# Performance work log

Hardware: AMD Instinct MI355X
Metric: run time of the kernel (lower is better)

## Reference

```python
import jax, jax.numpy as jnp
import numpy as np

NUM_HEADS = 8
EMBED_DIM = 512
HEAD_SIZE = EMBED_DIM // NUM_HEADS
B, S = 4, 2048


def setup_inputs() -> dict:
    key = jax.random.key(0)
    ks = jax.random.split(key, 9)
    scale = 1.0 / np.sqrt(HEAD_SIZE)
    return {
        "values": jax.random.normal(ks[0], (B, S, EMBED_DIM), jnp.float32),
        "keys": jax.random.normal(ks[1], (B, S, EMBED_DIM), jnp.float32),
        "query": jax.random.normal(ks[2], (B, S, EMBED_DIM), jnp.float32),
        "mask": jax.random.randint(ks[3], (B, S), 0, 2, jnp.int32),
        # per-head projection weights, nn.Linear convention: y = x @ W.T, W is [out,in]
        "Wv": jax.random.normal(ks[4], (HEAD_SIZE, HEAD_SIZE), jnp.float32) * scale,
        "Wk": jax.random.normal(ks[5], (HEAD_SIZE, HEAD_SIZE), jnp.float32) * scale,
        "Wq": jax.random.normal(ks[6], (HEAD_SIZE, HEAD_SIZE), jnp.float32) * scale,
        "Wo": jax.random.normal(ks[7], (EMBED_DIM, EMBED_DIM), jnp.float32) * (1.0 / np.sqrt(EMBED_DIM)),
        "bo": jax.random.normal(ks[8], (EMBED_DIM,), jnp.float32) * 0.01,
    }


def reference(values, keys, query, mask, Wv, Wk, Wq, Wo, bo):
    b, s, e = query.shape
    h, d = NUM_HEADS, HEAD_SIZE
    # reshape to heads, then shared per-head linear (no bias): x @ W.T
    v = jnp.einsum("bkhd,ed->bkhe", values.reshape(b, s, h, d), Wv)
    k = jnp.einsum("bkhd,ed->bkhe", keys.reshape(b, s, h, d), Wk)
    q = jnp.einsum("bqhd,ed->bqhe", query.reshape(b, s, h, d), Wq)
    # scores [b,h,q,k]
    energy = jnp.einsum("bqhd,bkhd->bhqk", q, k)
    energy = jnp.where(mask[:, None, None, :] == 0, jnp.float32(-1e20), energy)
    # NOTE: original scales by sqrt(embed_dim), not sqrt(head_size)
    attention = jax.nn.softmax(energy / np.sqrt(e).astype(np.float32), axis=3)
    out = jnp.einsum("bhqk,bkhd->bqhd", attention, v).reshape(b, s, e)
    out = out @ Wo.T + bo
    return out, attention
```

## Files before the change

kernel.cpp:

```cpp
#include <hip/hip_runtime.h>
#include <hip/hip_bf16.h>

#define Bn 4
#define Sn 2048
#define Hn 8
#define Dn 64
#define En 512

typedef __attribute__((ext_vector_type(8))) short short8v;
typedef __attribute__((ext_vector_type(4))) float float4v;

__device__ __forceinline__ short f2bf(float x){
    __hip_bfloat16 h = __float2bfloat16(x);
    return *reinterpret_cast<short*>(&h);
}
__device__ __forceinline__ float bf2f(short s){
    union { unsigned int u; float f; } c;
    c.u = ((unsigned int)(unsigned short)s) << 16;
    return c.f;
}

__global__ __launch_bounds__(256) void wo_cvt_kernel(const float* __restrict__ Wo,
                                                     short* __restrict__ Wob){
    int i = (blockIdx.x * 256 + threadIdx.x) * 4;
    float4 v = *(const float4*)(Wo + i);
    short4 o;
    o.x = f2bf(v.x); o.y = f2bf(v.y); o.z = f2bf(v.z); o.w = f2bf(v.w);
    *(short4*)(Wob + i) = o;
}

__global__ __launch_bounds__(256) void proj_kernel(
    const float* __restrict__ values, const float* __restrict__ keys, const float* __restrict__ query,
    const float* __restrict__ Wv, const float* __restrict__ Wk, const float* __restrict__ Wq,
    short* __restrict__ Qp, short* __restrict__ Kp, short* __restrict__ Vt)
{
    const int sel = blockIdx.z;
    const float* X = (sel == 0) ? values : ((sel == 1) ? keys : query);
    const float* W = (sel == 0) ? Wv : ((sel == 1) ? Wk : Wq);
    const int bh = blockIdx.y;
    const int b = bh >> 3, h = bh & 7;
    const int s0 = blockIdx.x * 64;
    const int wave = threadIdx.x >> 6;
    const int lane = threadIdx.x & 63;
    const int l16 = lane & 15, quad = lane >> 4;

    short8v bw[4][2];
    #pragma unroll
    for (int t = 0; t < 4; t++){
      #pragma unroll
      for (int st = 0; st < 2; st++){
        const float* wp = W + (t*16 + l16)*64 + st*32 + quad*8;
        float4 w0 = *(const float4*)(wp);
        float4 w1 = *(const float4*)(wp + 4);
        short8v f;
        f[0]=f2bf(w0.x); f[1]=f2bf(w0.y); f[2]=f2bf(w0.z); f[3]=f2bf(w0.w);
        f[4]=f2bf(w1.x); f[5]=f2bf(w1.y); f[6]=f2bf(w1.z); f[7]=f2bf(w1.w);
        bw[t][st] = f;
      }
    }

    const int row = s0 + wave*16 + l16;
    short8v fa[2];
    #pragma unroll
    for (int st = 0; st < 2; st++){
        const float* xp = X + ((size_t)b*Sn + row)*En + h*Dn + st*32 + quad*8;
        float4 x0 = *(const float4*)(xp);
        float4 x1 = *(const float4*)(xp + 4);
        short8v f;
        f[0]=f2bf(x0.x); f[1]=f2bf(x0.y); f[2]=f2bf(x0.z); f[3]=f2bf(x0.w);
        f[4]=f2bf(x1.x); f[5]=f2bf(x1.y); f[6]=f2bf(x1.z); f[7]=f2bf(x1.w);
        fa[st] = f;
    }

    const int rbase = s0 + wave*16 + quad*4;
    if (sel == 0){
        #pragma unroll
        for (int t = 0; t < 4; t++){
            float4v a = {0.f,0.f,0.f,0.f};
            a = __builtin_amdgcn_mfma_f32_16x16x32_bf16(fa[0], bw[t][0], a, 0,0,0);
            a = __builtin_amdgcn_mfma_f32_16x16x32_bf16(fa[1], bw[t][1], a, 0,0,0);
            int e = t*16 + l16;
            short4 pk;
            pk.x = f2bf(a[0]); pk.y = f2bf(a[1]); pk.z = f2bf(a[2]); pk.w = f2bf(a[3]);
            *(short4*)(Vt + ((size_t)bh*Dn + e)*Sn + rbase) = pk;
        }
    } else {
        short* dst = (sel == 1) ? Kp : Qp;
        #pragma unroll
        for (int t = 0; t < 4; t++){
            float4v a = {0.f,0.f,0.f,0.f};
            a = __builtin_amdgcn_mfma_f32_16x16x32_bf16(fa[0], bw[t][0], a, 0,0,0);
            a = __builtin_amdgcn_mfma_f32_16x16x32_bf16(fa[1], bw[t][1], a, 0,0,0);
            int e = t*16 + l16;
            #pragma unroll
            for (int r = 0; r < 4; r++)
                dst[((size_t)bh*Sn + rbase + r)*Dn + e] = f2bf(a[r]);
        }
    }
}

__global__ __launch_bounds__(256) void attn_kernel(
    const short* __restrict__ Qp, const short* __restrict__ Kp, const short* __restrict__ Vt,
    const int* __restrict__ mask, float* __restrict__ attn, short* __restrict__ Obf)
{
    __shared__ short sc[16][2056];
    __shared__ float wsum[4][16];
    __shared__ float vinv[16];

    const int qt = blockIdx.x, h = blockIdx.y, b = blockIdx.z;
    const int bh = b*Hn + h;
    const int tid = threadIdx.x;
    const int wave = tid >> 6, lane = tid & 63;
    const int l16 = lane & 15, quad = lane >> 4;
    const int q0 = qt * 16;

    const short* Qbase = Qp + (size_t)bh*Sn*Dn;
    const short* Kbase = Kp + (size_t)bh*Sn*Dn;
    const short* Vbase = Vt + (size_t)bh*Dn*Sn;

    short8v qa0 = *(const short8v*)(Qbase + (q0 + l16)*Dn + quad*8);
    short8v qa1 = *(const short8v*)(Qbase + (q0 + l16)*Dn + 32 + quad*8);

    const float SCALE = 0.0441941738241592f;
    float rs0=0.f, rs1=0.f, rs2=0.f, rs3=0.f;
    const int kw = wave * 512;
    const int km = b*Sn;
    for (int t = 0; t < 32; t++){
        const int k0 = kw + t*16;
        short8v kb0 = *(const short8v*)(Kbase + (k0 + l16)*Dn + quad*8);
        short8v kb1 = *(const short8v*)(Kbase + (k0 + l16)*Dn + 32 + quad*8);
        float4v a = {0.f,0.f,0.f,0.f};
        a = __builtin_amdgcn_mfma_f32_16x16x32_bf16(qa0, kb0, a, 0,0,0);
        a = __builtin_amdgcn_mfma_f32_16x16x32_bf16(qa1, kb1, a, 0,0,0);
        const int mk = mask[km + k0 + l16];
        const int col = k0 + l16;
        float p0 = (mk != 0) ? __expf(a[0]*SCALE) : 0.f;
        float p1 = (mk != 0) ? __expf(a[1]*SCALE) : 0.f;
        float p2 = (mk != 0) ? __expf(a[2]*SCALE) : 0.f;
        float p3 = (mk != 0) ? __expf(a[3]*SCALE) : 0.f;
        rs0 += p0; rs1 += p1; rs2 += p2; rs3 += p3;
        sc[quad*4 + 0][col] = f2bf(p0);
        sc[quad*4 + 1][col] = f2bf(p1);
        sc[quad*4 + 2][col] = f2bf(p2);
        sc[quad*4 + 3][col] = f2bf(p3);
    }
    #pragma unroll
    for (int off = 1; off < 16; off <<= 1){
        rs0 += __shfl_xor(rs0, off);
        rs1 += __shfl_xor(rs1, off);
        rs2 += __shfl_xor(rs2, off);
        rs3 += __shfl_xor(rs3, off);
    }
    if (l16 == 0){
        wsum[wave][quad*4 + 0] = rs0;
        wsum[wave][quad*4 + 1] = rs1;
        wsum[wave][quad*4 + 2] = rs2;
        wsum[wave][quad*4 + 3] = rs3;
    }
    __syncthreads();
    if (tid < 16){
        float s = wsum[0][tid] + wsum[1][tid] + wsum[2][tid] + wsum[3][tid];
        vinv[tid] = (s > 0.f) ? 1.f/s : 0.f;
    }
    __syncthreads();

    float* arow = attn + (size_t)bh*Sn*Sn + (size_t)q0*Sn;
    for (int row = 0; row < 16; row++){
        const float sr = vinv[row];
        short8v v8 = *(const short8v*)(&sc[row][tid*8]);
        float4v o0, o1;
        o0[0]=bf2f(v8[0])*sr; o0[1]=bf2f(v8[1])*sr; o0[2]=bf2f(v8[2])*sr; o0[3]=bf2f(v8[3])*sr;
        o1[0]=bf2f(v8[4])*sr; o1[1]=bf2f(v8[5])*sr; o1[2]=bf2f(v8[6])*sr; o1[3]=bf2f(v8[7])*sr;
        float* dst = arow + (size_t)row*Sn + tid*8;
        __builtin_nontemporal_store(o0, (float4v*)dst);
        __builtin_nontemporal_store(o1, (float4v*)(dst + 4));
    }

    float4v oacc0 = {0.f,0.f,0.f,0.f}, oacc1 = {0.f,0.f,0.f,0.f},
            oacc2 = {0.f,0.f,0.f,0.f}, oacc3 = {0.f,0.f,0.f,0.f};
    for (int ks = 0; ks < 16; ks++){
        const int kb = kw + ks*32 + quad*8;
        short8v pa  = *(const short8v*)(&sc[l16][kb]);
        short8v vb0 = *(const short8v*)(Vbase + (size_t)( 0 + l16)*Sn + kb);
        short8v vb1 = *(const short8v*)(Vbase + (size_t)(16 + l16)*Sn + kb);
        short8v vb2 = *(const short8v*)(Vbase + (size_t)(32 + l16)*Sn + kb);
        short8v vb3 = *(const short8v*)(Vbase + (size_t)(48 + l16)*Sn + kb);
        oacc0 = __builtin_amdgcn_mfma_f32_16x16x32_bf16(pa, vb0, oacc0, 0,0,0);
        oacc1 = __builtin_amdgcn_mfma_f32_16x16x32_bf16(pa, vb1, oacc1, 0,0,0);
        oacc2 = __builtin_amdgcn_mfma_f32_16x16x32_bf16(pa, vb2, oacc2, 0,0,0);
        oacc3 = __builtin_amdgcn_mfma_f32_16x16x32_bf16(pa, vb3, oacc3, 0,0,0);
    }
    __syncthreads();
    float* osc = (float*)&sc[0][0];
    {
        const int rb = quad*4;
        #pragma unroll
        for (int r = 0; r < 4; r++){
            osc[wave*1024 + (rb + r)*64 +  0 + l16] = oacc0[r];
            osc[wave*1024 + (rb + r)*64 + 16 + l16] = oacc1[r];
            osc[wave*1024 + (rb + r)*64 + 32 + l16] = oacc2[r];
            osc[wave*1024 + (rb + r)*64 + 48 + l16] = oacc3[r];
        }
    }
    __syncthreads();
    #pragma unroll
    for (int i = 0; i < 4; i++){
        const int id = tid + i*256;
        const int row = id >> 6, d = id & 63;
        float v = osc[id] + osc[1024 + id] + osc[2048 + id] + osc[3072 + id];
        v *= vinv[row];
        Obf[((size_t)b*Sn + q0 + row)*En + h*Dn + d] = f2bf(v);
    }
}

__global__ __launch_bounds__(256) void outproj_kernel(
    const short* __restrict__ Obf, const short* __restrict__ Wob,
    const float* __restrict__ bo, float* __restrict__ out)
{
    const int nt = blockIdx.x;
    const int mt = blockIdx.y;
    const int wave = threadIdx.x >> 6, lane = threadIdx.x & 63;
    const int l16 = lane & 15, quad = lane >> 4;
    const int m0 = mt*64 + wave*16;
    const int n0 = nt*64;

    float4v acc0 = {0.f,0.f,0.f,0.f}, acc1 = {0.f,0.f,0.f,0.f},
            acc2 = {0.f,0.f,0.f,0.f}, acc3 = {0.f,0.f,0.f,0.f};
    for (int ks = 0; ks < 16; ks++){
        const int kb = ks*32 + quad*8;
        short8v af = *(const short8v*)(Obf + (size_t)(m0 + l16)*En + kb);
        short8v b0 = *(const short8v*)(Wob + (size_t)(n0 +  0 + l16)*En + kb);
        short8v b1 = *(const short8v*)(Wob + (size_t)(n0 + 16 + l16)*En + kb);
        short8v b2 = *(const short8v*)(Wob + (size_t)(n0 + 32 + l16)*En + kb);
        short8v b3 = *(const short8v*)(Wob + (size_t)(n0 + 48 + l16)*En + kb);
        acc0 = __builtin_amdgcn_mfma_f32_16x16x32_bf16(af, b0, acc0, 0,0,0);
        acc1 = __builtin_amdgcn_mfma_f32_16x16x32_bf16(af, b1, acc1, 0,0,0);
        acc2 = __builtin_amdgcn_mfma_f32_16x16x32_bf16(af, b2, acc2, 0,0,0);
        acc3 = __builtin_amdgcn_mfma_f32_16x16x32_bf16(af, b3, acc3, 0,0,0);
    }
    #pragma unroll
    for (int t = 0; t < 4; t++){
        float4v a = (t==0)?acc0:((t==1)?acc1:((t==2)?acc2:acc3));
        const int e = n0 + t*16 + l16;
        const float bias = bo[e];
        #pragma unroll
        for (int r = 0; r < 4; r++)
            out[(size_t)(m0 + quad*4 + r)*En + e] = a[r] + bias;
    }
}

extern "C" void kernel_launch(void* const* d_in, const int* in_sizes, int n_in,
                              void* d_out, int out_size, void* d_ws, size_t ws_size,
                              hipStream_t stream)
{
    const float* values = (const float*)d_in[0];
    const float* keys   = (const float*)d_in[1];
    const float* query  = (const float*)d_in[2];
    const int*   mask   = (const int*)d_in[3];
    const float* Wv = (const float*)d_in[4];
    const float* Wk = (const float*)d_in[5];
    const float* Wq = (const float*)d_in[6];
    const float* Wo = (const float*)d_in[7];
    const float* bo = (const float*)d_in[8];

    float* out  = (float*)d_out;
    float* attn = out + (size_t)Bn*Sn*En;

    short* Qp  = (short*)d_ws;
    short* Kp  = Qp + (size_t)Bn*Hn*Sn*Dn;
    short* Vt  = Kp + (size_t)Bn*Hn*Sn*Dn;
    short* Obf = Vt + (size_t)Bn*Hn*Sn*Dn;
    short* Wob = Obf + (size_t)Bn*Sn*En;

    wo_cvt_kernel<<<dim3((En*En)/1024), 256, 0, stream>>>(Wo, Wob);
    proj_kernel<<<dim3(Sn/64, Bn*Hn, 3), 256, 0, stream>>>(values, keys, query, Wv, Wk, Wq, Qp, Kp, Vt);
    attn_kernel<<<dim3(Sn/16, Hn, Bn), 256, 0, stream>>>(Qp, Kp, Vt, mask, attn, Obf);
    outproj_kernel<<<dim3(En/64, (Bn*Sn)/64), 256, 0, stream>>>(Obf, Wob, bo, out);
}
```

Before: 863.3 us.

## Keep attention probabilities in registers and shrink LDS to raise occupancy

The attention kernel now computes the transposed score tile (K·Q), so each lane holds four consecutive key columns for one query row. The exponentials are kept packed as bf16 in registers rather than in a 16x2048 LDS buffer. Attention rows are written straight from registers as float4 stores, and the probabilities are staged through a small per-wave LDS tile in two chunks for the P·V MFMA. LDS use drops from about 64KB to about 33KB, with launch bounds asking for 3 blocks per CU, and the projection kernel now writes Q/K as packed short4 stores. The trade-off is a full 32-step unroll holding 64 packed registers per lane, which raises register pressure and risks spills.

```diff
diff --git a/kernel.cpp b/kernel.cpp
--- a/kernel.cpp
+++ b/kernel.cpp
@@ -9,6 +9,7 @@
 
 typedef __attribute__((ext_vector_type(8))) short short8v;
 typedef __attribute__((ext_vector_type(4))) float float4v;
+typedef __attribute__((ext_vector_type(2))) unsigned int uint2v;
 
 __device__ __forceinline__ short f2bf(float x){
     __hip_bfloat16 h = __float2bfloat16(x);
@@ -18,6 +19,9 @@
     union { unsigned int u; float f; } c;
     c.u = ((unsigned int)(unsigned short)s) << 16;
     return c.f;
+}
+__device__ __forceinline__ unsigned int pack2(float lo, float hi){
+    return (unsigned int)(unsigned short)f2bf(lo) | ((unsigned int)(unsigned short)f2bf(hi) << 16);
 }
 
 __global__ __launch_bounds__(256) void wo_cvt_kernel(const float* __restrict__ Wo,
@@ -72,8 +76,8 @@
         fa[st] = f;
     }
 
-    const int rbase = s0 + wave*16 + quad*4;
     if (sel == 0){
+        const int rbase = s0 + wave*16 + quad*4;
         #pragma unroll
         for (int t = 0; t < 4; t++){
             float4v a = {0.f,0.f,0.f,0.f};
@@ -89,21 +93,20 @@
         #pragma unroll
         for (int t = 0; t < 4; t++){
             float4v a = {0.f,0.f,0.f,0.f};
-            a = __builtin_amdgcn_mfma_f32_16x16x32_bf16(fa[0], bw[t][0], a, 0,0,0);
-            a = __builtin_amdgcn_mfma_f32_16x16x32_bf16(fa[1], bw[t][1], a, 0,0,0);
-            int e = t*16 + l16;
-            #pragma unroll
-            for (int r = 0; r < 4; r++)
-                dst[((size_t)bh*Sn + rbase + r)*Dn + e] = f2bf(a[r]);
-        }
-    }
-}
-
-__global__ __launch_bounds__(256) void attn_kernel(
+            a = __builtin_amdgcn_mfma_f32_16x16x32_bf16(bw[t][0], fa[0], a, 0,0,0);
+            a = __builtin_amdgcn_mfma_f32_16x16x32_bf16(bw[t][1], fa[1], a, 0,0,0);
+            short4 pk;
+            pk.x = f2bf(a[0]); pk.y = f2bf(a[1]); pk.z = f2bf(a[2]); pk.w = f2bf(a[3]);
+            *(short4*)(dst + ((size_t)bh*Sn + row)*Dn + t*16 + quad*4) = pk;
+        }
+    }
+}
+
+__global__ __launch_bounds__(256, 3) void attn_kernel(
     const short* __restrict__ Qp, const short* __restrict__ Kp, const short* __restrict__ Vt,
     const int* __restrict__ mask, float* __restrict__ attn, short* __restrict__ Obf)
 {
-    __shared__ short sc[16][2056];
+    __shared__ short sc[4][16][264];
     __shared__ float wsum[4][16];
     __shared__ float vinv[16];
 
@@ -122,94 +125,95 @@
     short8v qa1 = *(const short8v*)(Qbase + (q0 + l16)*Dn + 32 + quad*8);
 
     const float SCALE = 0.0441941738241592f;
-    float rs0=0.f, rs1=0.f, rs2=0.f, rs3=0.f;
     const int kw = wave * 512;
     const int km = b*Sn;
+
+    unsigned int pk[32][2];
+    float rs = 0.f;
+    #pragma unroll
     for (int t = 0; t < 32; t++){
         const int k0 = kw + t*16;
         short8v kb0 = *(const short8v*)(Kbase + (k0 + l16)*Dn + quad*8);
         short8v kb1 = *(const short8v*)(Kbase + (k0 + l16)*Dn + 32 + quad*8);
         float4v a = {0.f,0.f,0.f,0.f};
-        a = __builtin_amdgcn_mfma_f32_16x16x32_bf16(qa0, kb0, a, 0,0,0);
-        a = __builtin_amdgcn_mfma_f32_16x16x32_bf16(qa1, kb1, a, 0,0,0);
-        const int mk = mask[km + k0 + l16];
-        const int col = k0 + l16;
-        float p0 = (mk != 0) ? __expf(a[0]*SCALE) : 0.f;
-        float p1 = (mk != 0) ? __expf(a[1]*SCALE) : 0.f;
-        float p2 = (mk != 0) ? __expf(a[2]*SCALE) : 0.f;
-        float p3 = (mk != 0) ? __expf(a[3]*SCALE) : 0.f;
-        rs0 += p0; rs1 += p1; rs2 += p2; rs3 += p3;
-        sc[quad*4 + 0][col] = f2bf(p0);
-        sc[quad*4 + 1][col] = f2bf(p1);
-        sc[quad*4 + 2][col] = f2bf(p2);
-        sc[quad*4 + 3][col] = f2bf(p3);
-    }
-    #pragma unroll
-    for (int off = 1; off < 16; off <<= 1){
-        rs0 += __shfl_xor(rs0, off);
-        rs1 += __shfl_xor(rs1, off);
-        rs2 += __shfl_xor(rs2, off);
-        rs3 += __shfl_xor(rs3, off);
-    }
-    if (l16 == 0){
-        wsum[wave][quad*4 + 0] = rs0;
-        wsum[wave][quad*4 + 1] = rs1;
-        wsum[wave][quad*4 + 2] = rs2;
-        wsum[wave][quad*4 + 3] = rs3;
-    }
+        a = __builtin_amdgcn_mfma_f32_16x16x32_bf16(kb0, qa0, a, 0,0,0);
+        a = __builtin_amdgcn_mfma_f32_16x16x32_bf16(kb1, qa1, a, 0,0,0);
+        const int4 mk = *(const int4*)(mask + km + k0 + quad*4);
+        float p0 = mk.x ? __expf(a[0]*SCALE) : 0.f;
+        float p1 = mk.y ? __expf(a[1]*SCALE) : 0.f;
+        float p2 = mk.z ? __expf(a[2]*SCALE) : 0.f;
+        float p3 = mk.w ? __expf(a[3]*SCALE) : 0.f;
+        rs += (p0 + p1) + (p2 + p3);
+        pk[t][0] = pack2(p0, p1);
+        pk[t][1] = pack2(p2, p3);
+    }
+
+    rs += __shfl_xor(rs, 16);
+    rs += __shfl_xor(rs, 32);
+    if (lane < 16) wsum[wave][lane] = rs;
     __syncthreads();
-    if (tid < 16){
-        float s = wsum[0][tid] + wsum[1][tid] + wsum[2][tid] + wsum[3][tid];
-        vinv[tid] = (s > 0.f) ? 1.f/s : 0.f;
-    }
+    const float stot = wsum[0][l16] + wsum[1][l16] + wsum[2][l16] + wsum[3][l16];
+    const float vq = (stot > 0.f) ? 1.f/stot : 0.f;
+    if (tid < 16) vinv[tid] = vq;
+
+    float* arow = attn + (size_t)bh*Sn*Sn + (size_t)(q0 + l16)*Sn + kw + quad*4;
+    #pragma unroll
+    for (int t = 0; t < 32; t++){
+        float4v o;
+        o[0] = bf2f((short)(pk[t][0] & 0xffff)) * vq;
+        o[1] = bf2f((short)(pk[t][0] >> 16))    * vq;
+        o[2] = bf2f((short)(pk[t][1] & 0xffff)) * vq;
+        o[3] = bf2f((short)(pk[t][1] >> 16))    * vq;
+        __builtin_nontemporal_store(o, (float4v*)(arow + t*16));
+    }
+
+    float4v acc0 = {0.f,0.f,0.f,0.f}, acc1 = {0.f,0.f,0.f,0.f},
+            acc2 = {0.f,0.f,0.f,0.f}, acc3 = {0.f,0.f,0.f,0.f};
+    short* scw = &sc[wave][0][0];
+    #pragma unroll
+    for (int c = 0; c < 2; c++){
+        #pragma unroll
+        for (int tc = 0; tc < 16; tc++){
+            uint2v w2;
+            w2[0] = pk[c*16 + tc][0];
+            w2[1] = pk[c*16 + tc][1];
+            *(uint2v*)(scw + l16*264 + tc*16 + quad*4) = w2;
+        }
+        #pragma unroll
+        for (int ks = 0; ks < 8; ks++){
+            const int kv = kw + c*256 + ks*32 + quad*8;
+            short8v pa  = *(const short8v*)(scw + l16*264 + ks*32 + quad*8);
+            short8v vb0 = *(const short8v*)(Vbase + (size_t)( 0 + l16)*Sn + kv);
+            short8v vb1 = *(const short8v*)(Vbase + (size_t)(16 + l16)*Sn + kv);
+            short8v vb2 = *(const short8v*)(Vbase + (size_t)(32 + l16)*Sn + kv);
+            short8v vb3 = *(const short8v*)(Vbase + (size_t)(48 + l16)*Sn + kv);
+            acc0 = __builtin_amdgcn_mfma_f32_16x16x32_bf16(vb0, pa, acc0, 0,0,0);
+            acc1 = __builtin_amdgcn_mfma_f32_16x16x32_bf16(vb1, pa, acc1, 0,0,0);
+            acc2 = __builtin_amdgcn_mfma_f32_16x16x32_bf16(vb2, pa, acc2, 0,0,0);
+            acc3 = __builtin_amdgcn_mfma_f32_16x16x32_bf16(vb3, pa, acc3, 0,0,0);
+        }
+    }
+
     __syncthreads();
-
-    float* arow = attn + (size_t)bh*Sn*Sn + (size_t)q0*Sn;
-    for (int row = 0; row < 16; row++){
-        const float sr = vinv[row];
-        short8v v8 = *(const short8v*)(&sc[row][tid*8]);
-        float4v o0, o1;
-        o0[0]=bf2f(v8[0])*sr; o0[1]=bf2f(v8[1])*sr; o0[2]=bf2f(v8[2])*sr; o0[3]=bf2f(v8[3])*sr;
-        o1[0]=bf2f(v8[4])*sr; o1[1]=bf2f(v8[5])*sr; o1[2]=bf2f(v8[6])*sr; o1[3]=bf2f(v8[7])*sr;
-        float* dst = arow + (size_t)row*Sn + tid*8;
-        __builtin_nontemporal_store(o0, (float4v*)dst);
-        __builtin_nontemporal_store(o1, (float4v*)(dst + 4));
-    }
-
-    float4v oacc0 = {0.f,0.f,0.f,0.f}, oacc1 = {0.f,0.f,0.f,0.f},
-            oacc2 = {0.f,0.f,0.f,0.f}, oacc3 = {0.f,0.f,0.f,0.f};
-    for (int ks = 0; ks < 16; ks++){
-        const int kb = kw + ks*32 + quad*8;
-        short8v pa  = *(const short8v*)(&sc[l16][kb]);
-        short8v vb0 = *(const short8v*)(Vbase + (size_t)( 0 + l16)*Sn + kb);
-        short8v vb1 = *(const short8v*)(Vbase + (size_t)(16 + l16)*Sn + kb);
-        short8v vb2 = *(const short8v*)(Vbase + (size_t)(32 + l16)*Sn + kb);
-        short8v vb3 = *(const short8v*)(Vbase + (size_t)(48 + l16)*Sn + kb);
-        oacc0 = __builtin_amdgcn_mfma_f32_16x16x32_bf16(pa, vb0, oacc0, 0,0,0);
-        oacc1 = __builtin_amdgcn_mfma_f32_16x16x32_bf16(pa, vb1, oacc1, 0,0,0);
-        oacc2 = __builtin_amdgcn_mfma_f32_16x16x32_bf16(pa, vb2, oacc2, 0,0,0);
-        oacc3 = __builtin_amdgcn_mfma_f32_16x16x32_bf16(pa, vb3, oacc3, 0,0,0);
+    float* osc = (float*)&sc[0][0][0];
+    {
+        float* orow = osc + (wave*16 + l16)*68 + quad*4;
+        *(float4v*)(orow +  0) = acc0;
+        *(float4v*)(orow + 16) = acc1;
+        *(float4v*)(orow + 32) = acc2;
+        *(float4v*)(orow + 48) = acc3;
     }
     __syncthreads();
-    float* osc = (float*)&sc[0][0];
     {
-        const int rb = quad*4;
-        #pragma unroll
-        for (int r = 0; r < 4; r++){
-            osc[wave*1024 + (rb + r)*64 +  0 + l16] = oacc0[r];
-            osc[wave*1024 + (rb + r)*64 + 16 + l16] = oacc1[r];
-            osc[wave*1024 + (rb + r)*64 + 32 + l16] = oacc2[r];
-            osc[wave*1024 + (rb + r)*64 + 48 + l16] = oacc3[r];
-        }
-    }
-    __syncthreads();
-    #pragma unroll
-    for (int i = 0; i < 4; i++){
-        const int id = tid + i*256;
-        const int row = id >> 6, d = id & 63;
-        float v = osc[id] + osc[1024 + id] + osc[2048 + id] + osc[3072 + id];
-        v *= vinv[row];
-        Obf[((size_t)b*Sn + q0 + row)*En + h*Dn + d] = f2bf(v);
+        const int row = tid >> 4, dbase = (tid & 15)*4;
+        float4v v =  *(const float4v*)(osc + ( 0 + row)*68 + dbase);
+        v = v + *(const float4v*)(osc + (16 + row)*68 + dbase);
+        v = v + *(const float4v*)(osc + (32 + row)*68 + dbase);
+        v = v + *(const float4v*)(osc + (48 + row)*68 + dbase);
+        const float s = vinv[row];
+        short4 o;
+        o.x = f2bf(v[0]*s); o.y = f2bf(v[1]*s); o.z = f2bf(v[2]*s); o.w = f2bf(v[3]*s);
+        *(short4*)(Obf + ((size_t)b*Sn + q0 + row)*En + h*Dn + dbase) = o;
     }
 }
 
```

New measurement: 882.2 us. 1.02x slower.
